# Kernel optimization log

Measured on AMD Instinct MI355X. Metric: run time of the kernel, lower is better.

Reference implementation:

```python
import jax, jax.numpy as jnp
import numpy as np
import math

N, E = 10000, 640000
IN, HID, OUT, EF = 64, 64, 64, 16


def setup_inputs() -> dict:
    key = jax.random.key(0)
    ks = jax.random.split(key, 16)
    def lin(k, fan_in, fan_out):
        return jax.random.normal(k, (fan_in, fan_out), jnp.float32) / np.sqrt(fan_in)
    return {
        "node_feat": jax.random.normal(ks[0], (N, IN), jnp.float32),
        "coord_feat": jax.random.normal(ks[1], (N, 3), jnp.float32),
        "edge_feat": jax.random.normal(ks[2], (E, EF), jnp.float32),
        "W_e1": lin(ks[3], 2 * IN + EF + 1, HID), "b_e1": jnp.zeros((HID,), jnp.float32),
        "W_e2": lin(ks[4], HID, HID), "b_e2": jnp.zeros((HID,), jnp.float32),
        "W_n1": lin(ks[5], IN + HID, HID), "b_n1": jnp.zeros((HID,), jnp.float32),
        "W_n2": lin(ks[6], HID, OUT), "b_n2": jnp.zeros((OUT,), jnp.float32),
        "W_q": lin(ks[7], IN, HID),
        "W_k": lin(ks[8], IN + EF + 1, HID),
        "src": jax.random.randint(ks[9], (E,), 0, N, jnp.int32),
        "dst": jax.random.randint(ks[10], (E,), 0, N, jnp.int32),
    }


def reference(node_feat, coord_feat, edge_feat,
              W_e1, b_e1, W_e2, b_e2, W_n1, b_n1, W_n2, b_n2,
              W_q, W_k, src, dst):
    silu = jax.nn.silu
    # per-edge gathers
    h_src = node_feat[src]                      # [E, IN]
    h_dst = node_feat[dst]                      # [E, IN]
    x_diff = coord_feat[src] - coord_feat[dst]  # [E, 3]
    dist = jnp.sqrt(jnp.sum(x_diff * x_diff, axis=1, keepdims=True))  # [E, 1]
    # edge MLP message
    f = jnp.concatenate([h_src, h_dst, dist, edge_feat], axis=-1)      # [E, 2*IN+1+EF]
    msg_h = silu(silu(f @ W_e1 + b_e1) @ W_e2 + b_e2)                  # [E, HID]
    # attention score (QK dot)
    k_raw = jnp.concatenate([h_src, dist, edge_feat], axis=-1)         # [E, IN+1+EF]
    msg_k = k_raw @ W_k                                                # [E, HID]
    msg_q = h_dst @ W_q                                                # [E, HID]
    e = jnp.sum(msg_k * msg_q, axis=-1) / math.sqrt(HID)               # [E]
    # segment softmax over incoming edges of each dst node
    e_max = jax.ops.segment_max(e, dst, num_segments=N)                # [N]
    e_exp = jnp.exp(e - e_max[dst])                                    # [E]
    denom = jax.ops.segment_sum(e_exp, dst, num_segments=N)            # [N]
    att = e_exp / denom[dst]                                           # [E]
    # attention-weighted scatter-sum aggregation
    h_neigh = jax.ops.segment_sum(msg_h * att[:, None], dst, num_segments=N)  # [N, HID]
    # node MLP
    h = silu(jnp.concatenate([node_feat, h_neigh], axis=-1) @ W_n1 + b_n1) @ W_n2 + b_n2
    return h
```

## Files before the change

### kernel.cpp

```cpp
#include <hip/hip_runtime.h>

#define NN 10000
#define NE 640000

typedef __attribute__((ext_vector_type(8))) short bf16x8;
typedef __attribute__((ext_vector_type(4))) short s16x4;
typedef __attribute__((ext_vector_type(4))) float f32x4;

#define MFMA __builtin_amdgcn_mfma_f32_16x16x32_bf16

static __device__ __forceinline__ float silu_f(float x) {
    return x / (1.f + __expf(-x));
}
static __device__ __forceinline__ short f2bf(float x) {
    union { float f; unsigned u; } v; v.f = x;
    unsigned r = (v.u + 0x7FFF + ((v.u >> 16) & 1)) >> 16;
    return (short)r;
}

__global__ __launch_bounds__(256) void k_hist(const int* __restrict__ dst,
                                              int* __restrict__ cnt) {
    int e = blockIdx.x * 256 + threadIdx.x;
    if (e < NE) atomicAdd(&cnt[dst[e]], 1);
}

__global__ __launch_bounds__(256) void k_scan(const int* __restrict__ cnt,
                                              int* __restrict__ row_start,
                                              int* __restrict__ cursor) {
    __shared__ int part[256];
    __shared__ int base[257];
    const int t = threadIdx.x;
    int loc[40];
    int s = 0;
    #pragma unroll
    for (int i = 0; i < 40; i++) {
        int idx = t * 40 + i;
        int v = (idx < NN) ? cnt[idx] : 0;
        loc[i] = s; s += v;
    }
    part[t] = s;
    __syncthreads();
    if (t == 0) {
        int a = 0;
        for (int j = 0; j < 256; j++) { base[j] = a; a += part[j]; }
        base[256] = a;
    }
    __syncthreads();
    #pragma unroll
    for (int i = 0; i < 40; i++) {
        int idx = t * 40 + i;
        if (idx < NN) { int v = base[t] + loc[i]; row_start[idx] = v; cursor[idx] = v; }
    }
    if (t == 0) row_start[NN] = base[256];
}

__global__ __launch_bounds__(256) void k_scatter(
    const int* __restrict__ dst, const int* __restrict__ src,
    const float* __restrict__ node_feat, const float* __restrict__ ef,
    const float* __restrict__ coord,
    const float* __restrict__ G, const float* __restrict__ EQn,
    const float* __restrict__ WQn,
    int* __restrict__ cursor, int* __restrict__ src_s,
    unsigned short* __restrict__ dist_s, float* __restrict__ w_s,
    unsigned short* __restrict__ efs)
{
    int e = blockIdx.x * 256 + threadIdx.x;
    if (e >= NE) return;
    const int d = dst[e];
    const int s = src[e];
    const int p = atomicAdd(&cursor[d], 1);

    const float dx = coord[s*3+0] - coord[d*3+0];
    const float dy = coord[s*3+1] - coord[d*3+1];
    const float dz = coord[s*3+2] - coord[d*3+2];
    const float dist = sqrtf(dx*dx + dy*dy + dz*dz);

    float sc = dist * WQn[d];
    const float4* xp = (const float4*)(node_feat + (size_t)s*64);
    const float4* gp = (const float4*)(G + (size_t)d*64);
    #pragma unroll
    for (int j = 0; j < 16; j++) {
        float4 a = xp[j], b = gp[j];
        sc += a.x*b.x + a.y*b.y + a.z*b.z + a.w*b.w;
    }
    const float4* ep = (const float4*)(ef + (size_t)e*16);
    const float4* qp = (const float4*)(EQn + (size_t)d*16);
    #pragma unroll
    for (int j = 0; j < 4; j++) {
        float4 a = ep[j], b = qp[j];
        sc += a.x*b.x + a.y*b.y + a.z*b.z + a.w*b.w;
        s16x4 p4;
        p4[0] = f2bf(a.x); p4[1] = f2bf(a.y); p4[2] = f2bf(a.z); p4[3] = f2bf(a.w);
        *(s16x4*)&efs[(size_t)p*16 + j*4] = p4;
    }
    w_s[p] = __expf(sc * 0.125f);
    src_s[p] = s;
    dist_s[p] = (unsigned short)f2bf(dist);
}

__global__ __launch_bounds__(256) void node_pre_kernel(
    const float* __restrict__ node_feat,
    const float* __restrict__ W_e1,
    const float* __restrict__ W_k,
    const float* __restrict__ W_q,
    short* __restrict__ nfb, float* __restrict__ B,
    float* __restrict__ G, float* __restrict__ EQn, float* __restrict__ WQn)
{
    __shared__ float sW1b[64*64];
    __shared__ float sWq[64*64];
    __shared__ float sWk[64*65];
    __shared__ float sWke[16*65];
    __shared__ __align__(16) float sx[4][64];
    __shared__ __align__(16) float sq[4][64];

    for (int i = threadIdx.x; i < 64*64; i += 256) {
        sW1b[i] = W_e1[64*64 + i];
        sWq[i]  = W_q[i];
        int c = i >> 6, j = i & 63;
        sWk[c*65 + j] = W_k[i];
    }
    for (int i = threadIdx.x; i < 16*64; i += 256) {
        int k = i >> 6, j = i & 63;
        sWke[k*65 + j] = W_k[(65 + k)*64 + j];
    }
    __syncthreads();

    const int wid = threadIdx.x >> 6;
    const int lane = threadIdx.x & 63;
    for (int n = blockIdx.x * 4 + wid; n < NN; n += gridDim.x * 4) {
        float x = node_feat[n*64 + lane];
        nfb[n*64 + lane] = f2bf(x);
        sx[wid][lane] = x;
        float b = 0.f, q = 0.f;
        #pragma unroll
        for (int i = 0; i < 64; i += 4) {
            float4 x4 = *(const float4*)&sx[wid][i];
            b += x4.x*sW1b[(i+0)*64+lane] + x4.y*sW1b[(i+1)*64+lane]
               + x4.z*sW1b[(i+2)*64+lane] + x4.w*sW1b[(i+3)*64+lane];
            q += x4.x*sWq[(i+0)*64+lane] + x4.y*sWq[(i+1)*64+lane]
               + x4.z*sWq[(i+2)*64+lane] + x4.w*sWq[(i+3)*64+lane];
        }
        B[n*64 + lane] = b;
        sq[wid][lane] = q;

        float g = 0.f;
        #pragma unroll
        for (int j = 0; j < 64; j += 4) {
            float4 q4 = *(const float4*)&sq[wid][j];
            g += q4.x*sWk[lane*65 + j]   + q4.y*sWk[lane*65 + j+1]
               + q4.z*sWk[lane*65 + j+2] + q4.w*sWk[lane*65 + j+3];
        }
        G[n*64 + lane] = g;

        float p = W_k[64*64 + lane] * q;
        #pragma unroll
        for (int off = 32; off; off >>= 1) p += __shfl_xor(p, off);
        if (lane == 0) WQn[n] = p;

        int kk = lane & 15, pp = lane >> 4;
        float s = 0.f;
        #pragma unroll
        for (int jj = 0; jj < 16; jj++) {
            int j = pp*16 + jj;
            s += sWke[kk*65 + j] * sq[wid][j];
        }
        s += __shfl_xor(s, 16); s += __shfl_xor(s, 32);
        if (lane < 16) EQn[n*16 + kk] = s;
    }
}

__global__ __launch_bounds__(512, 2) void edge_kernel(
    const short* __restrict__ nfb, const int* __restrict__ src_s,
    const unsigned short* __restrict__ dist_s, const float* __restrict__ w_s,
    const unsigned short* __restrict__ efs, const int* __restrict__ row_start,
    const float* __restrict__ W_e1, const float* __restrict__ b_e1,
    const float* __restrict__ W_e2, const float* __restrict__ b_e2,
    const float* __restrict__ B, float* __restrict__ hout)
{
    __shared__ short sW1T[64*104];
    __shared__ short sW2T[64*72];
    __shared__ short sX[8][16*104];
    __shared__ short sH1[8][16*72];

    const int tid = threadIdx.x;
    const int wid = tid >> 6, l = tid & 63;
    const int cl = l & 15, rg = l >> 4;
    const int er = l >> 2, q = l & 3;

    for (int i = tid; i < 64*104; i += 512) sW1T[i] = 0;
    __syncthreads();
    for (int i = tid; i < 64*82; i += 512) {
        int k = i >> 6, c = i & 63;
        float v;
        if (k < 64)       v = W_e1[k*64 + c];
        else if (k < 80)  v = W_e1[(129 + k - 64)*64 + c];
        else if (k == 80) v = W_e1[128*64 + c];
        else              v = b_e1[c];
        sW1T[c*104 + k] = f2bf(v);
    }
    for (int i = tid; i < 64*64; i += 512) {
        int k = i >> 6, c = i & 63;
        sW2T[c*72 + k] = f2bf(W_e2[k*64 + c]);
    }
    if (l < 16) {
        #pragma unroll
        for (int c = 82; c < 96; c++) sX[wid][l*104 + c] = 0;
        sX[wid][l*104 + 81] = (short)0x3F80;
    }
    __syncthreads();

    const int n = blockIdx.x * 8 + wid;
    const int beg = row_start[n], end = row_start[n+1];

    const size_t nb = (size_t)n*64;
    const float Bb0 = B[nb+cl],     Bb1 = B[nb+16+cl];
    const float Bb2 = B[nb+32+cl],  Bb3 = B[nb+48+cl];
    const float b20 = b_e2[cl],     b21 = b_e2[16+cl];
    const float b22 = b_e2[32+cl],  b23 = b_e2[48+cl];

    float hs0 = 0.f, hs1 = 0.f, hs2 = 0.f, hs3 = 0.f, den = 0.f;

    int idx = beg + er; if (idx > NE-1) idx = NE-1;
    int sN = src_s[idx];
    bf16x8 nfAN = *(const bf16x8*)&nfb[(size_t)sN*64 + q*8];
    bf16x8 nfBN = *(const bf16x8*)&nfb[(size_t)sN*64 + 32 + q*8];
    s16x4  efN  = *(const s16x4*)&efs[(size_t)idx*16 + q*4];
    unsigned short dN = dist_s[idx];
    float wvN[4];
    #pragma unroll
    for (int r = 0; r < 4; r++) {
        int j = beg + rg*4 + r;
        wvN[r] = (j < NE) ? w_s[j] : 0.f;
    }

    for (int c0 = beg; c0 < end; c0 += 16) {
        bf16x8 nfA = nfAN, nfB = nfBN; s16x4 ef4 = efN;
        unsigned short dcur = dN;
        float wv[4];
        #pragma unroll
        for (int r = 0; r < 4; r++) wv[r] = wvN[r];

        int idx2 = c0 + 16 + er; if (idx2 > NE-1) idx2 = NE-1;
        sN = src_s[idx2];
        nfAN = *(const bf16x8*)&nfb[(size_t)sN*64 + q*8];
        nfBN = *(const bf16x8*)&nfb[(size_t)sN*64 + 32 + q*8];
        efN  = *(const s16x4*)&efs[(size_t)idx2*16 + q*4];
        dN   = dist_s[idx2];
        #pragma unroll
        for (int r = 0; r < 4; r++) {
            int j = c0 + 16 + rg*4 + r;
            wvN[r] = (j < NE) ? w_s[j] : 0.f;
        }

        *(bf16x8*)&sX[wid][er*104 + q*8]      = nfA;
        *(bf16x8*)&sX[wid][er*104 + 32 + q*8] = nfB;
        *(s16x4*)&sX[wid][er*104 + 64 + q*4]  = ef4;
        if (q == 0) sX[wid][er*104 + 80] = (short)dcur;

        bf16x8 ax0 = *(const bf16x8*)&sX[wid][cl*104 +  0 + rg*8];
        bf16x8 ax1 = *(const bf16x8*)&sX[wid][cl*104 + 32 + rg*8];
        bf16x8 ax2 = *(const bf16x8*)&sX[wid][cl*104 + 64 + rg*8];
        f32x4 a0 = {Bb0,Bb0,Bb0,Bb0}, a1 = {Bb1,Bb1,Bb1,Bb1};
        f32x4 a2 = {Bb2,Bb2,Bb2,Bb2}, a3 = {Bb3,Bb3,Bb3,Bb3};
        a0 = MFMA(ax0, *(const bf16x8*)&sW1T[( 0+cl)*104 +  0 + rg*8], a0, 0,0,0);
        a0 = MFMA(ax1, *(const bf16x8*)&sW1T[( 0+cl)*104 + 32 + rg*8], a0, 0,0,0);
        a0 = MFMA(ax2, *(const bf16x8*)&sW1T[( 0+cl)*104 + 64 + rg*8], a0, 0,0,0);
        a1 = MFMA(ax0, *(const bf16x8*)&sW1T[(16+cl)*104 +  0 + rg*8], a1, 0,0,0);
        a1 = MFMA(ax1, *(const bf16x8*)&sW1T[(16+cl)*104 + 32 + rg*8], a1, 0,0,0);
        a1 = MFMA(ax2, *(const bf16x8*)&sW1T[(16+cl)*104 + 64 + rg*8], a1, 0,0,0);
        a2 = MFMA(ax0, *(const bf16x8*)&sW1T[(32+cl)*104 +  0 + rg*8], a2, 0,0,0);
        a2 = MFMA(ax1, *(const bf16x8*)&sW1T[(32+cl)*104 + 32 + rg*8], a2, 0,0,0);
        a2 = MFMA(ax2, *(const bf16x8*)&sW1T[(32+cl)*104 + 64 + rg*8], a2, 0,0,0);
        a3 = MFMA(ax0, *(const bf16x8*)&sW1T[(48+cl)*104 +  0 + rg*8], a3, 0,0,0);
        a3 = MFMA(ax1, *(const bf16x8*)&sW1T[(48+cl)*104 + 32 + rg*8], a3, 0,0,0);
        a3 = MFMA(ax2, *(const bf16x8*)&sW1T[(48+cl)*104 + 64 + rg*8], a3, 0,0,0);
        #pragma unroll
        for (int r = 0; r < 4; r++) {
            int row = rg*4 + r;
            sH1[wid][row*72 +  0 + cl] = f2bf(silu_f(a0[r]));
            sH1[wid][row*72 + 16 + cl] = f2bf(silu_f(a1[r]));
            sH1[wid][row*72 + 32 + cl] = f2bf(silu_f(a2[r]));
            sH1[wid][row*72 + 48 + cl] = f2bf(silu_f(a3[r]));
        }

        bf16x8 ah0 = *(const bf16x8*)&sH1[wid][cl*72 + rg*8];
        bf16x8 ah1 = *(const bf16x8*)&sH1[wid][cl*72 + 32 + rg*8];
        f32x4 c0v = {b20,b20,b20,b20}, c1v = {b21,b21,b21,b21};
        f32x4 c2v = {b22,b22,b22,b22}, c3v = {b23,b23,b23,b23};
        c0v = MFMA(ah0, *(const bf16x8*)&sW2T[( 0+cl)*72 +      rg*8], c0v, 0,0,0);
        c0v = MFMA(ah1, *(const bf16x8*)&sW2T[( 0+cl)*72 + 32 + rg*8], c0v, 0,0,0);
        c1v = MFMA(ah0, *(const bf16x8*)&sW2T[(16+cl)*72 +      rg*8], c1v, 0,0,0);
        c1v = MFMA(ah1, *(const bf16x8*)&sW2T[(16+cl)*72 + 32 + rg*8], c1v, 0,0,0);
        c2v = MFMA(ah0, *(const bf16x8*)&sW2T[(32+cl)*72 +      rg*8], c2v, 0,0,0);
        c2v = MFMA(ah1, *(const bf16x8*)&sW2T[(32+cl)*72 + 32 + rg*8], c2v, 0,0,0);
        c3v = MFMA(ah0, *(const bf16x8*)&sW2T[(48+cl)*72 +      rg*8], c3v, 0,0,0);
        c3v = MFMA(ah1, *(const bf16x8*)&sW2T[(48+cl)*72 + 32 + rg*8], c3v, 0,0,0);

        #pragma unroll
        for (int r = 0; r < 4; r++) {
            float wr = (c0 + rg*4 + r < end) ? wv[r] : 0.f;
            hs0 += wr * silu_f(c0v[r]);
            hs1 += wr * silu_f(c1v[r]);
            hs2 += wr * silu_f(c2v[r]);
            hs3 += wr * silu_f(c3v[r]);
            den += wr;
        }
    }

    hs0 += __shfl_xor(hs0, 16); hs0 += __shfl_xor(hs0, 32);
    hs1 += __shfl_xor(hs1, 16); hs1 += __shfl_xor(hs1, 32);
    hs2 += __shfl_xor(hs2, 16); hs2 += __shfl_xor(hs2, 32);
    hs3 += __shfl_xor(hs3, 16); hs3 += __shfl_xor(hs3, 32);
    den += __shfl_xor(den, 16); den += __shfl_xor(den, 32);

    float v = (rg == 0) ? hs0 : (rg == 1) ? hs1 : (rg == 2) ? hs2 : hs3;
    hout[nb + l] = (den > 0.f) ? v / den : 0.f;
}

__global__ __launch_bounds__(256) void node_out_kernel(
    const float* __restrict__ node_feat,
    const float* __restrict__ W_n1, const float* __restrict__ b_n1,
    const float* __restrict__ W_n2, const float* __restrict__ b_n2,
    const float* __restrict__ hacc, float* __restrict__ out)
{
    __shared__ float sWn1[128*64];
    __shared__ float sWn2[64*64];
    __shared__ __align__(16) float sx[4][64], sg[4][64], st[4][64];

    for (int i = threadIdx.x; i < 128*64; i += 256) sWn1[i] = W_n1[i];
    for (int i = threadIdx.x; i < 64*64; i += 256)  sWn2[i] = W_n2[i];
    __syncthreads();

    const int wid = threadIdx.x >> 6;
    const int lane = threadIdx.x & 63;
    for (int n = blockIdx.x * 4 + wid; n < NN; n += gridDim.x * 4) {
        sx[wid][lane] = node_feat[n*64 + lane];
        sg[wid][lane] = hacc[n*64 + lane];

        float acc = b_n1[lane];
        #pragma unroll
        for (int i = 0; i < 64; i += 4) {
            float4 x4 = *(const float4*)&sx[wid][i];
            float4 g4 = *(const float4*)&sg[wid][i];
            acc += x4.x*sWn1[(i+0)*64+lane] + x4.y*sWn1[(i+1)*64+lane]
                 + x4.z*sWn1[(i+2)*64+lane] + x4.w*sWn1[(i+3)*64+lane];
            acc += g4.x*sWn1[(64+i+0)*64+lane] + g4.y*sWn1[(64+i+1)*64+lane]
                 + g4.z*sWn1[(64+i+2)*64+lane] + g4.w*sWn1[(64+i+3)*64+lane];
        }
        const float tt = silu_f(acc);
        st[wid][lane] = tt;

        float acc2 = b_n2[lane];
        #pragma unroll
        for (int i = 0; i < 64; i += 4) {
            float4 t4 = *(const float4*)&st[wid][i];
            acc2 += t4.x*sWn2[(i+0)*64+lane] + t4.y*sWn2[(i+1)*64+lane]
                  + t4.z*sWn2[(i+2)*64+lane] + t4.w*sWn2[(i+3)*64+lane];
        }
        out[n*64 + lane] = acc2;
    }
}

extern "C" void kernel_launch(void* const* d_in, const int* in_sizes, int n_in,
                              void* d_out, int out_size, void* d_ws, size_t ws_size,
                              hipStream_t stream) {
    const float* node_feat = (const float*)d_in[0];
    const float* coord     = (const float*)d_in[1];
    const float* edge_feat = (const float*)d_in[2];
    const float* W_e1 = (const float*)d_in[3];
    const float* b_e1 = (const float*)d_in[4];
    const float* W_e2 = (const float*)d_in[5];
    const float* b_e2 = (const float*)d_in[6];
    const float* W_n1 = (const float*)d_in[7];
    const float* b_n1 = (const float*)d_in[8];
    const float* W_n2 = (const float*)d_in[9];
    const float* b_n2 = (const float*)d_in[10];
    const float* W_q  = (const float*)d_in[11];
    const float* W_k  = (const float*)d_in[12];
    const int* src = (const int*)d_in[13];
    const int* dst = (const int*)d_in[14];
    float* out = (float*)d_out;

    float* ws = (float*)d_ws;
    short* nfb       = (short*)ws;
    float* B         = ws + 320000;
    float* G         = ws + 960000;
    float* hacc      = ws + 960000;
    float* EQn       = ws + 1600000;
    float* WQn       = ws + 1760000;
    int*   cnt       = (int*)(ws + 1770000);
    int*   row_start = (int*)(ws + 1780000);
    int*   cursor    = (int*)(ws + 1790004);
    int*   src_s     = (int*)(ws + 1800004);
    float* w_s       = ws + 2440004;
    unsigned short* dist_s = (unsigned short*)(ws + 3080004);
    unsigned short* efs    = (unsigned short*)(ws + 3400004);

    hipMemsetAsync(cnt, 0, NN * sizeof(int), stream);

    node_pre_kernel<<<625, 256, 0, stream>>>(node_feat, W_e1, W_k, W_q,
                                             nfb, B, G, EQn, WQn);
    k_hist<<<2500, 256, 0, stream>>>(dst, cnt);
    k_scan<<<1, 256, 0, stream>>>(cnt, row_start, cursor);
    k_scatter<<<2500, 256, 0, stream>>>(dst, src, node_feat, edge_feat, coord,
                                        G, EQn, WQn, cursor,
                                        src_s, dist_s, w_s, efs);
    edge_kernel<<<1250, 512, 0, stream>>>(nfb, src_s, dist_s, w_s, efs, row_start,
                                          W_e1, b_e1, W_e2, b_e2, B, hacc);
    node_out_kernel<<<625, 256, 0, stream>>>(node_feat, W_n1, b_n1, W_n2, b_n2,
                                             hacc, out);
}
```

Measured before the change: 425.9 us.

## Move attention score into edge kernel and split scatter into permute plus pack

The attention logit per edge is no longer computed in the scatter kernel, where each edge read fp32 node_feat[src] and G[dst] rows at random addresses. It is now computed inside edge_kernel from the bf16 source features already loaded there, with G and EQn staged in shared memory per destination. The scatter is split into an atomic permutation pass and a separate pack pass whose scattered writes become sequential. This adds one launch and a perm buffer, and the score now uses bf16-rounded inputs, which lowers precision.

```diff
diff --git a/kernel.cpp b/kernel.cpp
--- a/kernel.cpp
+++ b/kernel.cpp
@@ -16,6 +16,10 @@
     union { float f; unsigned u; } v; v.f = x;
     unsigned r = (v.u + 0x7FFF + ((v.u >> 16) & 1)) >> 16;
     return (short)r;
+}
+static __device__ __forceinline__ float bf2f(short h) {
+    union { float f; unsigned u; } v; v.u = ((unsigned)(unsigned short)h) << 16;
+    return v.f;
 }
 
 __global__ __launch_bounds__(256) void k_hist(const int* __restrict__ dst,
@@ -54,48 +58,46 @@
     if (t == 0) row_start[NN] = base[256];
 }
 
-__global__ __launch_bounds__(256) void k_scatter(
-    const int* __restrict__ dst, const int* __restrict__ src,
-    const float* __restrict__ node_feat, const float* __restrict__ ef,
+__global__ __launch_bounds__(256) void k_scatter(const int* __restrict__ dst,
+                                                 int* __restrict__ cursor,
+                                                 int* __restrict__ perm) {
+    int e = blockIdx.x * 256 + threadIdx.x;
+    if (e < NE) {
+        int d = dst[e];
+        int p = atomicAdd(&cursor[d], 1);
+        perm[p] = e;
+    }
+}
+
+__global__ __launch_bounds__(256) void k_pack(
+    const int* __restrict__ perm, const int* __restrict__ src,
+    const int* __restrict__ dst, const float* __restrict__ ef,
     const float* __restrict__ coord,
-    const float* __restrict__ G, const float* __restrict__ EQn,
-    const float* __restrict__ WQn,
-    int* __restrict__ cursor, int* __restrict__ src_s,
-    unsigned short* __restrict__ dist_s, float* __restrict__ w_s,
+    int* __restrict__ src_s, unsigned short* __restrict__ dist_s,
     unsigned short* __restrict__ efs)
 {
-    int e = blockIdx.x * 256 + threadIdx.x;
-    if (e >= NE) return;
+    int p = blockIdx.x * 256 + threadIdx.x;
+    if (p >= NE) return;
+    const int e = perm[p];
+    const int s = src[e];
     const int d = dst[e];
-    const int s = src[e];
-    const int p = atomicAdd(&cursor[d], 1);
 
     const float dx = coord[s*3+0] - coord[d*3+0];
     const float dy = coord[s*3+1] - coord[d*3+1];
     const float dz = coord[s*3+2] - coord[d*3+2];
     const float dist = sqrtf(dx*dx + dy*dy + dz*dz);
 
-    float sc = dist * WQn[d];
-    const float4* xp = (const float4*)(node_feat + (size_t)s*64);
-    const float4* gp = (const float4*)(G + (size_t)d*64);
-    #pragma unroll
-    for (int j = 0; j < 16; j++) {
-        float4 a = xp[j], b = gp[j];
-        sc += a.x*b.x + a.y*b.y + a.z*b.z + a.w*b.w;
-    }
+    src_s[p] = s;
+    dist_s[p] = (unsigned short)f2bf(dist);
+
     const float4* ep = (const float4*)(ef + (size_t)e*16);
-    const float4* qp = (const float4*)(EQn + (size_t)d*16);
     #pragma unroll
     for (int j = 0; j < 4; j++) {
-        float4 a = ep[j], b = qp[j];
-        sc += a.x*b.x + a.y*b.y + a.z*b.z + a.w*b.w;
+        float4 a = ep[j];
         s16x4 p4;
         p4[0] = f2bf(a.x); p4[1] = f2bf(a.y); p4[2] = f2bf(a.z); p4[3] = f2bf(a.w);
         *(s16x4*)&efs[(size_t)p*16 + j*4] = p4;
     }
-    w_s[p] = __expf(sc * 0.125f);
-    src_s[p] = s;
-    dist_s[p] = (unsigned short)f2bf(dist);
 }
 
 __global__ __launch_bounds__(256) void node_pre_kernel(
@@ -171,16 +173,20 @@
 
 __global__ __launch_bounds__(512, 2) void edge_kernel(
     const short* __restrict__ nfb, const int* __restrict__ src_s,
-    const unsigned short* __restrict__ dist_s, const float* __restrict__ w_s,
+    const unsigned short* __restrict__ dist_s,
     const unsigned short* __restrict__ efs, const int* __restrict__ row_start,
     const float* __restrict__ W_e1, const float* __restrict__ b_e1,
     const float* __restrict__ W_e2, const float* __restrict__ b_e2,
-    const float* __restrict__ B, float* __restrict__ hout)
+    const float* __restrict__ B, const float* __restrict__ G,
+    const float* __restrict__ EQn, const float* __restrict__ WQn,
+    float* __restrict__ hout)
 {
     __shared__ short sW1T[64*104];
     __shared__ short sW2T[64*72];
     __shared__ short sX[8][16*104];
     __shared__ short sH1[8][16*72];
+    __shared__ __align__(16) float sG[8][64];
+    __shared__ __align__(16) float sEQ[8][16];
 
     const int tid = threadIdx.x;
     const int wid = tid >> 6, l = tid & 63;
@@ -217,6 +223,9 @@
     const float Bb2 = B[nb+32+cl],  Bb3 = B[nb+48+cl];
     const float b20 = b_e2[cl],     b21 = b_e2[16+cl];
     const float b22 = b_e2[32+cl],  b23 = b_e2[48+cl];
+    sG[wid][l] = G[nb + l];
+    if (l < 16) sEQ[wid][l] = EQn[(size_t)n*16 + l];
+    const float wq = WQn[n];
 
     float hs0 = 0.f, hs1 = 0.f, hs2 = 0.f, hs3 = 0.f, den = 0.f;
 
@@ -226,19 +235,10 @@
     bf16x8 nfBN = *(const bf16x8*)&nfb[(size_t)sN*64 + 32 + q*8];
     s16x4  efN  = *(const s16x4*)&efs[(size_t)idx*16 + q*4];
     unsigned short dN = dist_s[idx];
-    float wvN[4];
-    #pragma unroll
-    for (int r = 0; r < 4; r++) {
-        int j = beg + rg*4 + r;
-        wvN[r] = (j < NE) ? w_s[j] : 0.f;
-    }
 
     for (int c0 = beg; c0 < end; c0 += 16) {
         bf16x8 nfA = nfAN, nfB = nfBN; s16x4 ef4 = efN;
         unsigned short dcur = dN;
-        float wv[4];
-        #pragma unroll
-        for (int r = 0; r < 4; r++) wv[r] = wvN[r];
 
         int idx2 = c0 + 16 + er; if (idx2 > NE-1) idx2 = NE-1;
         sN = src_s[idx2];
@@ -246,11 +246,19 @@
         nfBN = *(const bf16x8*)&nfb[(size_t)sN*64 + 32 + q*8];
         efN  = *(const s16x4*)&efs[(size_t)idx2*16 + q*4];
         dN   = dist_s[idx2];
-        #pragma unroll
-        for (int r = 0; r < 4; r++) {
-            int j = c0 + 16 + rg*4 + r;
-            wvN[r] = (j < NE) ? w_s[j] : 0.f;
-        }
+
+        const float dist = bf2f((short)dcur);
+        float p_ = 0.f;
+        #pragma unroll
+        for (int i = 0; i < 8; i++) {
+            p_ += bf2f(nfA[i]) * sG[wid][q*8 + i];
+            p_ += bf2f(nfB[i]) * sG[wid][32 + q*8 + i];
+        }
+        #pragma unroll
+        for (int i = 0; i < 4; i++)
+            p_ += bf2f(ef4[i]) * sEQ[wid][q*4 + i];
+        p_ += __shfl_xor(p_, 1); p_ += __shfl_xor(p_, 2);
+        const float wgt = __expf((p_ + dist * wq) * 0.125f);
 
         *(bf16x8*)&sX[wid][er*104 + q*8]      = nfA;
         *(bf16x8*)&sX[wid][er*104 + 32 + q*8] = nfB;
@@ -298,7 +306,8 @@
 
         #pragma unroll
         for (int r = 0; r < 4; r++) {
-            float wr = (c0 + rg*4 + r < end) ? wv[r] : 0.f;
+            int row = rg*4 + r;
+            float wr = (c0 + row < end) ? __shfl(wgt, row << 2) : 0.f;
             hs0 += wr * silu_f(c0v[r]);
             hs1 += wr * silu_f(c1v[r]);
             hs2 += wr * silu_f(c2v[r]);
@@ -385,16 +394,16 @@
     short* nfb       = (short*)ws;
     float* B         = ws + 320000;
     float* G         = ws + 960000;
-    float* hacc      = ws + 960000;
     float* EQn       = ws + 1600000;
     float* WQn       = ws + 1760000;
     int*   cnt       = (int*)(ws + 1770000);
     int*   row_start = (int*)(ws + 1780000);
     int*   cursor    = (int*)(ws + 1790004);
-    int*   src_s     = (int*)(ws + 1800004);
-    float* w_s       = ws + 2440004;
+    int*   perm      = (int*)(ws + 1800004);
+    int*   src_s     = (int*)(ws + 2440004);
     unsigned short* dist_s = (unsigned short*)(ws + 3080004);
     unsigned short* efs    = (unsigned short*)(ws + 3400004);
+    float* hacc      = ws + 8520004;
 
     hipMemsetAsync(cnt, 0, NN * sizeof(int), stream);
 
@@ -402,11 +411,12 @@
                                              nfb, B, G, EQn, WQn);
     k_hist<<<2500, 256, 0, stream>>>(dst, cnt);
     k_scan<<<1, 256, 0, stream>>>(cnt, row_start, cursor);
-    k_scatter<<<2500, 256, 0, stream>>>(dst, src, node_feat, edge_feat, coord,
-                                        G, EQn, WQn, cursor,
-                                        src_s, dist_s, w_s, efs);
-    edge_kernel<<<1250, 512, 0, stream>>>(nfb, src_s, dist_s, w_s, efs, row_start,
-                                          W_e1, b_e1, W_e2, b_e2, B, hacc);
+    k_scatter<<<2500, 256, 0, stream>>>(dst, cursor, perm);
+    k_pack<<<2500, 256, 0, stream>>>(perm, src, dst, edge_feat, coord,
+                                     src_s, dist_s, efs);
+    edge_kernel<<<1250, 512, 0, stream>>>(nfb, src_s, dist_s, efs, row_start,
+                                          W_e1, b_e1, W_e2, b_e2,
+                                          B, G, EQn, WQn, hacc);
     node_out_kernel<<<625, 256, 0, stream>>>(node_feat, W_n1, b_n1, W_n2, b_n2,
                                              hacc, out);
 }
```

Measured after the change: 367.3 us. 13.8% less time.
